# Performance work log

Measured on AMD Instinct MI355X. Metric: run time of the kernel, lower is better.

Reference implementation:

```python
import jax, jax.numpy as jnp
import numpy as np

L, C = 32768, 512
EPS = 1e-5

def _layernorm(x, w, b):
    mu = jnp.mean(x, axis=-1, keepdims=True)
    var = jnp.mean(jnp.square(x - mu), axis=-1, keepdims=True)
    return (x - mu) * jax.lax.rsqrt(var + EPS) * w + b

def _scan(u, decay):
    # inclusive first-order linear scan: b_t = decay * b_{t-1} + u_t
    a = jnp.broadcast_to(decay, u.shape)
    def combine(l, r):
        return (l[0] * r[0], r[1] + r[0] * l[1])
    _, b = jax.lax.associative_scan(combine, (a, u), axis=0)
    return b

def setup_inputs() -> dict:
    key = jax.random.key(0)
    ks = jax.random.split(key, 8)
    s = 0.02
    return {
        "x": jax.random.normal(ks[0], (L, C), dtype=jnp.float32),
        "ln1_w": jnp.ones((C,), jnp.float32),
        "ln1_b": jnp.zeros((C,), jnp.float32),
        "W_in": jax.random.normal(ks[1], (C, C), jnp.float32) * s,
        "b_in": jnp.zeros((C,), jnp.float32),
        "W_gate": jax.random.normal(ks[2], (C, C), jnp.float32) * s,
        "b_gate": jnp.zeros((C,), jnp.float32),
        "W_out": jax.random.normal(ks[3], (C, C), jnp.float32) * s,
        "b_out": jnp.zeros((C,), jnp.float32),
        "decay_logit": jnp.zeros((C,), jnp.float32),  # torch init: zeros -> sigmoid = 0.5
        "ln2_w": jnp.ones((C,), jnp.float32),
        "ln2_b": jnp.zeros((C,), jnp.float32),
        "W_ff1": jax.random.normal(ks[4], (C, 2 * C), jnp.float32) * s,
        "b_ff1": jnp.zeros((2 * C,), jnp.float32),
        "W_ff2": jax.random.normal(ks[5], (2 * C, C), jnp.float32) * s,
        "b_ff2": jnp.zeros((C,), jnp.float32),
    }

def reference(x, ln1_w, ln1_b, W_in, b_in, W_gate, b_gate, W_out, b_out,
              decay_logit, ln2_w, ln2_b, W_ff1, b_ff1, W_ff2, b_ff2):
    hidden = _layernorm(x, ln1_w, ln1_b)
    u = hidden @ W_in + b_in
    gate = jax.nn.sigmoid(hidden @ W_gate + b_gate)
    decay = jax.nn.sigmoid(decay_logit)
    fwd = _scan(u, decay) * gate
    bwd = jnp.flip(_scan(jnp.flip(u, axis=0), decay), axis=0) * gate
    state_out = 0.5 * (fwd + bwd)
    x = x + state_out @ W_out + b_out
    h = _layernorm(x, ln2_w, ln2_b)
    x = x + jax.nn.silu(h @ W_ff1 + b_ff1) @ W_ff2 + b_ff2
    return x
```

## Files before the change

### kernel.cpp

```cpp
#include <hip/hip_runtime.h>
#include <stdint.h>


#define L_SEQ 32768
#define CDIM 512
#define LN_EPS 1e-5f
#define CHUNK 64
#define NCHUNK (L_SEQ / CHUNK)

typedef __attribute__((ext_vector_type(8))) short short8;
typedef __attribute__((ext_vector_type(4))) float floatx4;

__device__ inline unsigned short f2bf(float f) {
  union { float f; unsigned int u; } v; v.f = f;
  unsigned int r = v.u + 0x7fffu + ((v.u >> 16) & 1u);
  return (unsigned short)(r >> 16);
}
__device__ inline float bf2f(unsigned short h) {
  union { float f; unsigned int u; } v; v.u = ((unsigned int)h) << 16;
  return v.f;
}
__device__ inline float sigmoidf_(float x) { return 1.0f / (1.0f + __expf(-x)); }

__device__ __forceinline__ void gll16(const void* g, void* l) {
  __builtin_amdgcn_global_load_lds(
      (__attribute__((address_space(1))) void*)g,
      (__attribute__((address_space(3))) void*)l, 16, 0, 0);
}

__global__ __launch_bounds__(256) void ln_kernel(const float* __restrict__ x,
    const float* __restrict__ w, const float* __restrict__ b,
    unsigned short* __restrict__ out) {
  int row = blockIdx.x * 4 + (threadIdx.x >> 6);
  int lane = threadIdx.x & 63;
  const float4* xr = (const float4*)(x + (size_t)row * CDIM);
  float4 v0 = xr[lane * 2];
  float4 v1 = xr[lane * 2 + 1];
  float s = v0.x + v0.y + v0.z + v0.w + v1.x + v1.y + v1.z + v1.w;
  float s2 = v0.x * v0.x + v0.y * v0.y + v0.z * v0.z + v0.w * v0.w +
             v1.x * v1.x + v1.y * v1.y + v1.z * v1.z + v1.w * v1.w;
  for (int m = 32; m > 0; m >>= 1) {
    s += __shfl_xor(s, m, 64);
    s2 += __shfl_xor(s2, m, 64);
  }
  float mean = s * (1.0f / CDIM);
  float var = s2 * (1.0f / CDIM) - mean * mean;
  float rs = rsqrtf(var + LN_EPS);
  const float4* wr = (const float4*)w;
  const float4* br = (const float4*)b;
  float4 w0 = wr[lane * 2], w1 = wr[lane * 2 + 1];
  float4 b0 = br[lane * 2], b1 = br[lane * 2 + 1];
  unsigned int p0 = (unsigned int)f2bf((v0.x - mean) * rs * w0.x + b0.x) |
                    ((unsigned int)f2bf((v0.y - mean) * rs * w0.y + b0.y) << 16);
  unsigned int p1 = (unsigned int)f2bf((v0.z - mean) * rs * w0.z + b0.z) |
                    ((unsigned int)f2bf((v0.w - mean) * rs * w0.w + b0.w) << 16);
  unsigned int p2 = (unsigned int)f2bf((v1.x - mean) * rs * w1.x + b1.x) |
                    ((unsigned int)f2bf((v1.y - mean) * rs * w1.y + b1.y) << 16);
  unsigned int p3 = (unsigned int)f2bf((v1.z - mean) * rs * w1.z + b1.z) |
                    ((unsigned int)f2bf((v1.w - mean) * rs * w1.w + b1.w) << 16);
  uint4 pk; pk.x = p0; pk.y = p1; pk.z = p2; pk.w = p3;
  *((uint4*)(out + (size_t)row * CDIM + lane * 8)) = pk;
}

__global__ __launch_bounds__(256) void prep_all(
    const float* __restrict__ W_in, const float* __restrict__ W_gate,
    const float* __restrict__ W_out, const float* __restrict__ W_ff1,
    const float* __restrict__ W_ff2, const float* __restrict__ logit,
    unsigned short* __restrict__ Wt_ig, unsigned short* __restrict__ Wt_out,
    unsigned short* __restrict__ Wt_ff1, unsigned short* __restrict__ Wt_ff2,
    float* __restrict__ decay, float* __restrict__ decayT) {
  int b = blockIdx.x;
  if (b >= 1792) {
    for (int c = threadIdx.x; c < CDIM; c += 256) {
      float d = sigmoidf_(logit[c]);
      decay[c] = d;
      float p = d;
      for (int i = 0; i < 6; i++) p *= p;
      decayT[c] = p;
    }
    return;
  }
  const float* W; unsigned short* Wt; int Kd, Nd, t;
  if (b < 256)       { W = W_in;   Wt = Wt_ig;             Kd = 512;  Nd = 512;  t = b; }
  else if (b < 512)  { W = W_gate; Wt = Wt_ig + 512 * 512; Kd = 512;  Nd = 512;  t = b - 256; }
  else if (b < 768)  { W = W_out;  Wt = Wt_out;            Kd = 512;  Nd = 512;  t = b - 512; }
  else if (b < 1280) { W = W_ff1;  Wt = Wt_ff1;            Kd = 512;  Nd = 1024; t = b - 768; }
  else               { W = W_ff2;  Wt = Wt_ff2;            Kd = 1024; Nd = 512;  t = b - 1280; }
  int ntx = Nd >> 5;
  int n0 = (t % ntx) * 32, k0 = (t / ntx) * 32;
  __shared__ float tile[32][33];
  int tx = threadIdx.x & 31, ty = threadIdx.x >> 5;
  for (int r = 0; r < 32; r += 8)
    tile[ty + r][tx] = W[(size_t)(k0 + ty + r) * Nd + n0 + tx];
  __syncthreads();
  for (int r = 0; r < 32; r += 8)
    Wt[(size_t)(n0 + ty + r) * Kd + k0 + tx] = f2bf(tile[tx][ty + r]);
}

template <int EPI>
__global__ __launch_bounds__(512, 2) void gemm256(
    const unsigned short* __restrict__ A, const unsigned short* __restrict__ Bt,
    const float* __restrict__ biasA, const float* __restrict__ biasB,
    const float* __restrict__ res, float* __restrict__ outF,
    unsigned short* __restrict__ outU, unsigned short* __restrict__ outG,
    int M, int N, int K) {
  __shared__ unsigned short smem[65536];
  unsigned short* As = smem;
  unsigned short* Bs = smem + 32768;

  int nbx = gridDim.x, nby = gridDim.y;
  int bid = blockIdx.x + blockIdx.y * nbx;
  int per = (nbx * nby) >> 3;
  int w = (bid & 7) * per + (bid >> 3);
  int ni = w % nby, mi = w / nby;
  int bm = mi << 8, bn = ni << 8;

  int tid = threadIdx.x, wave = tid >> 6, lane = tid & 63;
  int wm = (wave >> 2) * 128, wn = (wave & 3) * 64;
  int quad = lane >> 4, r16 = lane & 15;

  int sr = tid >> 2;
  int sc = tid & 3;
  int swz = (sr >> 1) & 3;
  const unsigned short* aSrc0 = A + (size_t)(bm + sr) * K + ((sc ^ swz) * 8);
  const unsigned short* aSrc1 = aSrc0 + (size_t)128 * K;
  const unsigned short* bSrc0 = Bt + (size_t)(bn + sr) * K + ((sc ^ swz) * 8);
  const unsigned short* bSrc1 = bSrc0 + (size_t)128 * K;
  int ldsW = wave * 512;

#define STAGE(slot, ktile) do {                                   \
    int _o = (ktile) * 32;                                        \
    unsigned short* _a = As + (slot) * 8192 + ldsW;               \
    unsigned short* _b = Bs + (slot) * 8192 + ldsW;               \
    gll16(aSrc0 + _o, _a);                                        \
    gll16(aSrc1 + _o, _a + 4096);                                 \
    gll16(bSrc0 + _o, _b);                                        \
    gll16(bSrc1 + _o, _b + 4096);                                 \
  } while (0)

  floatx4 acc[8][4];
#pragma unroll
  for (int i = 0; i < 8; i++)
#pragma unroll
    for (int j = 0; j < 4; j++) acc[i][j] = (floatx4){0.f, 0.f, 0.f, 0.f};

  int cOff = ((quad ^ ((r16 >> 1) & 3)) & 3) * 8;
  int aBase = (wm + r16) * 32 + cOff;
  int bBase = (wn + r16) * 32 + cOff;

  int NK = K >> 5;

  STAGE(0, 0); STAGE(1, 1); STAGE(2, 2);
  asm volatile("s_waitcnt vmcnt(8)" ::: "memory");
  __builtin_amdgcn_s_barrier();
  asm volatile("" ::: "memory");

  for (int j = 0; j < NK; ++j) {
    int slot = j & 3;
    if (j + 3 < NK) STAGE((j + 3) & 3, j + 3);
    const unsigned short* as = As + slot * 8192;
    const unsigned short* bs = Bs + slot * 8192;
    short8 af[8], bfr[4];
#pragma unroll
    for (int i = 0; i < 8; i++) af[i] = *(const short8*)(as + aBase + i * 512);
#pragma unroll
    for (int jj = 0; jj < 4; jj++) bfr[jj] = *(const short8*)(bs + bBase + jj * 512);
    if (j + 1 < NK) {
      asm volatile("s_waitcnt lgkmcnt(0)" ::: "memory");
      if (j + 3 < NK)      asm volatile("s_waitcnt vmcnt(8)" ::: "memory");
      else if (j + 2 < NK) asm volatile("s_waitcnt vmcnt(4)" ::: "memory");
      else                 asm volatile("s_waitcnt vmcnt(0)" ::: "memory");
      __builtin_amdgcn_s_barrier();
      asm volatile("" ::: "memory");
    }
    __builtin_amdgcn_s_setprio(1);
#pragma unroll
    for (int i = 0; i < 8; i++)
#pragma unroll
      for (int jj = 0; jj < 4; jj++)
        acc[i][jj] = __builtin_amdgcn_mfma_f32_16x16x32_bf16(af[i], bfr[jj], acc[i][jj], 0, 0, 0);
    __builtin_amdgcn_s_setprio(0);
  }
#undef STAGE

  if (EPI == 1) {
#pragma unroll
    for (int i = 0; i < 8; i++) {
      int mb = bm + wm + i * 16 + quad * 4;
#pragma unroll
      for (int jj = 0; jj < 4; jj++) {
        int n = bn + wn + jj * 16 + r16;
        float bA = biasA[n];
#pragma unroll
        for (int r = 0; r < 4; r++) {
          size_t idx = (size_t)(mb + r) * N + n;
          outF[idx] = res[idx] + acc[i][jj][r] + bA;
        }
      }
    }
  } else {
    unsigned short* sm16 = smem;
#define EPI_HALF(P) {                                                        \
      __syncthreads(); \
      _Pragma("unroll")                                                      \
      for (int jj = 0; jj < 4; jj++) {                                       \
        int colL = wn + jj * 16 + r16;                                       \
        int n = bn + colL;                                                   \
        _Pragma("unroll")                                                    \
        for (int i = 0; i < 4; i++) {                                        \
          int lr = (wm >> 1) + i * 16 + quad * 4;                            \
          _Pragma("unroll")                                                  \
          for (int r = 0; r < 4; r++) {                                      \
            float v = acc[(P) * 4 + i][jj][r];                               \
            float t;                                                         \
            if (EPI == 0) {                                                  \
              t = (n < 512) ? (v + biasA[n]) : sigmoidf_(v + biasB[n - 512]);\
            } else {                                           \
              float z = v + biasA[n];                                        \
              t = z * sigmoidf_(z);                                          \
            }                                                                \
            sm16[(lr + r) * 260 + colL] = f2bf(t);                           \
          }                                                                  \
        }                                                                    \
      }                                                                      \
      __syncthreads();                                                       \
      {                                                                      \
        int row = tid >> 2, c0 = (tid & 3) * 64;                             \
        int gr = bm + (row & 63) + ((row >> 6) * 128) + (P) * 64;            \
        const unsigned short* srcp = sm16 + row * 260 + c0;                  \
        unsigned short* gptr;                                                \
        if (EPI == 0) {                                                      \
          gptr = (bn < 512) ? (outU + (size_t)gr * 512 + bn + c0)            \
                            : (outG + (size_t)gr * 512 + (bn - 512) + c0);   \
        } else {                                                             \
          gptr = outG + (size_t)gr * N + bn + c0;                            \
        }                                                                    \
        _Pragma("unroll")                                                    \
        for (int s = 0; s < 8; s++)                                          \
          *(short8*)(gptr + s * 8) = *(const short8*)(srcp + s * 8);         \
      }                                                                      \
    }
    EPI_HALF(0)
    EPI_HALF(1)
#undef EPI_HALF
  }
}

__global__ __launch_bounds__(512) void scan_phase1(const unsigned short* __restrict__ u,
    const float* __restrict__ decay, float* __restrict__ fa, float* __restrict__ ba) {
  int c = threadIdx.x, k = blockIdx.x;
  float d = decay[c];
  const unsigned short* up = u + (size_t)k * CHUNK * CDIM + c;
  float f = 0.f, bs = 0.f, p = 1.f;
#pragma unroll 8
  for (int t = 0; t < CHUNK; t++) {
    float v = bf2f(up[(size_t)t * CDIM]);
    f = d * f + v;
    bs += p * v;
    p *= d;
  }
  fa[(size_t)k * CDIM + c] = f;
  ba[(size_t)k * CDIM + c] = bs;
}

__global__ __launch_bounds__(256) void scan_phase2(const float* __restrict__ fa,
    const float* __restrict__ ba, const float* __restrict__ decayT,
    float* __restrict__ fc, float* __restrict__ bc) {
  int c = blockIdx.x * 256 + threadIdx.x;
  float dT = decayT[c];
  float runf = 0.f, runb = 0.f;
#pragma unroll 4
  for (int k = 0; k < NCHUNK; k++) {
    int kb = NCHUNK - 1 - k;
    fc[(size_t)k * CDIM + c] = runf;
    runf = dT * runf + fa[(size_t)k * CDIM + c];
    bc[(size_t)kb * CDIM + c] = runb;
    runb = dT * runb + ba[(size_t)kb * CDIM + c];
  }
}

__global__ __launch_bounds__(512) void scan_phase3(const unsigned short* __restrict__ u,
    const unsigned short* __restrict__ gate, const float* __restrict__ decay,
    const float* __restrict__ fc, const float* __restrict__ bc,
    unsigned short* __restrict__ state) {
  int c = threadIdx.x, k = blockIdx.x;
  float d = decay[c];
  size_t base = (size_t)k * CHUNK * CDIM + c;
  float fwd[CHUNK];
  float run = fc[(size_t)k * CDIM + c];
#pragma unroll
  for (int t = 0; t < CHUNK; t++) {
    run = d * run + bf2f(u[base + (size_t)t * CDIM]);
    fwd[t] = run;
  }
  float runb = bc[(size_t)k * CDIM + c];
#pragma unroll
  for (int t = CHUNK - 1; t >= 0; t--) {
    runb = d * runb + bf2f(u[base + (size_t)t * CDIM]);
    float g = bf2f(gate[base + (size_t)t * CDIM]);
    state[base + (size_t)t * CDIM] = f2bf(0.5f * (fwd[t] + runb) * g);
  }
}

extern "C" void kernel_launch(void* const* d_in, const int* in_sizes, int n_in,
                              void* d_out, int out_size, void* d_ws, size_t ws_size,
                              hipStream_t stream) {
  const float* x = (const float*)d_in[0];
  const float* ln1_w = (const float*)d_in[1];
  const float* ln1_b = (const float*)d_in[2];
  const float* W_in = (const float*)d_in[3];
  const float* b_in = (const float*)d_in[4];
  const float* W_gate = (const float*)d_in[5];
  const float* b_gate = (const float*)d_in[6];
  const float* W_out = (const float*)d_in[7];
  const float* b_out = (const float*)d_in[8];
  const float* decay_logit = (const float*)d_in[9];
  const float* ln2_w = (const float*)d_in[10];
  const float* ln2_b = (const float*)d_in[11];
  const float* W_ff1 = (const float*)d_in[12];
  const float* b_ff1 = (const float*)d_in[13];
  const float* W_ff2 = (const float*)d_in[14];
  const float* b_ff2 = (const float*)d_in[15];

  char* ws = (char*)d_ws;
  size_t off = 0;
  auto alloc = [&](size_t bytes) -> void* {
    void* p = ws + off;
    off += (bytes + 255) & ~(size_t)255;
    return p;
  };
  unsigned short* Wt_ig  = (unsigned short*)alloc((size_t)1024 * 512 * 2);
  unsigned short* Wt_out = (unsigned short*)alloc((size_t)512 * 512 * 2);
  unsigned short* Wt_ff1 = (unsigned short*)alloc((size_t)1024 * 512 * 2);
  unsigned short* Wt_ff2 = (unsigned short*)alloc((size_t)512 * 1024 * 2);
  float* fa = (float*)alloc((size_t)NCHUNK * CDIM * 4);
  float* ba = (float*)alloc((size_t)NCHUNK * CDIM * 4);
  float* fc = (float*)alloc((size_t)NCHUNK * CDIM * 4);
  float* bc = (float*)alloc((size_t)NCHUNK * CDIM * 4);
  float* decay  = (float*)alloc(CDIM * 4);
  float* decayT = (float*)alloc(CDIM * 4);
  const size_t LC2 = (size_t)L_SEQ * CDIM * 2;
  unsigned short* R1 = (unsigned short*)alloc(LC2);
  unsigned short* R2 = (unsigned short*)alloc(LC2);
  unsigned short* R3 = (unsigned short*)alloc(LC2);
  unsigned short* hidden = R1;
  unsigned short* state  = R1;
  unsigned short* hbuf   = R1;
  unsigned short* u_buf  = R2;
  unsigned short* gate   = R3;
  unsigned short* ffb    = R2;
  float* x2 = (float*)d_out;

  prep_all<<<1793, 256, 0, stream>>>(W_in, W_gate, W_out, W_ff1, W_ff2,
      decay_logit, Wt_ig, Wt_out, Wt_ff1, Wt_ff2, decay, decayT);

  ln_kernel<<<L_SEQ / 4, 256, 0, stream>>>(x, ln1_w, ln1_b, hidden);

  gemm256<0><<<dim3(L_SEQ / 256, 1024 / 256), 512, 0, stream>>>(
      hidden, Wt_ig, b_in, b_gate, nullptr, nullptr, u_buf, gate, L_SEQ, 1024, 512);

  scan_phase1<<<NCHUNK, 512, 0, stream>>>(u_buf, decay, fa, ba);
  scan_phase2<<<2, 256, 0, stream>>>(fa, ba, decayT, fc, bc);
  scan_phase3<<<NCHUNK, 512, 0, stream>>>(u_buf, gate, decay, fc, bc, state);

  gemm256<1><<<dim3(L_SEQ / 256, 512 / 256), 512, 0, stream>>>(
      state, Wt_out, b_out, nullptr, x, x2, nullptr, nullptr, L_SEQ, 512, 512);

  ln_kernel<<<L_SEQ / 4, 256, 0, stream>>>(x2, ln2_w, ln2_b, hbuf);

  gemm256<2><<<dim3(L_SEQ / 256, 1024 / 256), 512, 0, stream>>>(
      hbuf, Wt_ff1, b_ff1, nullptr, nullptr, nullptr, nullptr, ffb, L_SEQ, 1024, 512);

  gemm256<1><<<dim3(L_SEQ / 256, 512 / 256), 512, 0, stream>>>(
      ffb, Wt_ff2, b_ff2, nullptr, x2, x2, nullptr, nullptr, L_SEQ, 512, 1024);
}
```

Before: 462.8 us.

## Interleave LDS reads, global prefetch, and MFMA groups in GEMM main loop

```diff
diff --git a/kernel.cpp b/kernel.cpp
--- a/kernel.cpp
+++ b/kernel.cpp
@@ -10,6 +10,7 @@
 
 typedef __attribute__((ext_vector_type(8))) short short8;
 typedef __attribute__((ext_vector_type(4))) float floatx4;
+typedef __attribute__((ext_vector_type(4))) int intx4;
 
 __device__ inline unsigned short f2bf(float f) {
   union { float f; unsigned int u; } v; v.f = f;
@@ -21,6 +22,9 @@
   return v.f;
 }
 __device__ inline float sigmoidf_(float x) { return 1.0f / (1.0f + __expf(-x)); }
+__device__ __forceinline__ short8 asS8(intx4 v) {
+  union { intx4 i; short8 s; } u; u.i = v; return u.s;
+}
 
 __device__ __forceinline__ void gll16(const void* g, void* l) {
   __builtin_amdgcn_global_load_lds(
@@ -128,7 +132,7 @@
   const unsigned short* bSrc1 = bSrc0 + (size_t)128 * K;
   int ldsW = wave * 512;
 
-#define STAGE(slot, ktile) do {                                   \
+#define STAGE4(slot, ktile) do {                                  \
     int _o = (ktile) * 32;                                        \
     unsigned short* _a = As + (slot) * 8192 + ldsW;               \
     unsigned short* _b = Bs + (slot) * 8192 + ldsW;               \
@@ -145,43 +149,91 @@
     for (int j = 0; j < 4; j++) acc[i][j] = (floatx4){0.f, 0.f, 0.f, 0.f};
 
   int cOff = ((quad ^ ((r16 >> 1) & 3)) & 3) * 8;
-  int aBase = (wm + r16) * 32 + cOff;
-  int bBase = (wn + r16) * 32 + cOff;
+  unsigned aByte = (unsigned)(((wm + r16) * 32 + cOff) * 2);
+  unsigned bByte = 65536u + (unsigned)(((wn + r16) * 32 + cOff) * 2);
 
   int NK = K >> 5;
 
-  STAGE(0, 0); STAGE(1, 1); STAGE(2, 2);
+#define DSR(dst, byteOff) asm volatile("ds_read_b128 %0, %1"              \
+    : "=v"(dst)                                                           \
+    : "v"((__attribute__((address_space(3))) const void*)                 \
+          ((const char*)smem + (byteOff))))
+
+#define LGKM0_FENCE() do {                                                \
+    asm volatile("s_waitcnt lgkmcnt(0)" ::: "memory");                    \
+    __builtin_amdgcn_sched_barrier(0);                                    \
+  } while (0)
+
+#define MFMA8(Q, A0, A1) do {                                             \
+    __builtin_amdgcn_s_setprio(1);                                        \
+    short8 _a0 = asS8(A0), _a1 = asS8(A1);                                \
+    short8 _b0 = asS8(tb0), _b1 = asS8(tb1), _b2 = asS8(tb2), _b3 = asS8(tb3); \
+    acc[2*(Q)  ][0] = __builtin_amdgcn_mfma_f32_16x16x32_bf16(_a0, _b0, acc[2*(Q)  ][0], 0, 0, 0); \
+    acc[2*(Q)  ][1] = __builtin_amdgcn_mfma_f32_16x16x32_bf16(_a0, _b1, acc[2*(Q)  ][1], 0, 0, 0); \
+    acc[2*(Q)  ][2] = __builtin_amdgcn_mfma_f32_16x16x32_bf16(_a0, _b2, acc[2*(Q)  ][2], 0, 0, 0); \
+    acc[2*(Q)  ][3] = __builtin_amdgcn_mfma_f32_16x16x32_bf16(_a0, _b3, acc[2*(Q)  ][3], 0, 0, 0); \
+    acc[2*(Q)+1][0] = __builtin_amdgcn_mfma_f32_16x16x32_bf16(_a1, _b0, acc[2*(Q)+1][0], 0, 0, 0); \
+    acc[2*(Q)+1][1] = __builtin_amdgcn_mfma_f32_16x16x32_bf16(_a1, _b1, acc[2*(Q)+1][1], 0, 0, 0); \
+    acc[2*(Q)+1][2] = __builtin_amdgcn_mfma_f32_16x16x32_bf16(_a1, _b2, acc[2*(Q)+1][2], 0, 0, 0); \
+    acc[2*(Q)+1][3] = __builtin_amdgcn_mfma_f32_16x16x32_bf16(_a1, _b3, acc[2*(Q)+1][3], 0, 0, 0); \
+    __builtin_amdgcn_s_setprio(0);                                        \
+  } while (0)
+
+  STAGE4(0, 0); STAGE4(1, 1); STAGE4(2, 2);
   asm volatile("s_waitcnt vmcnt(8)" ::: "memory");
   __builtin_amdgcn_s_barrier();
-  asm volatile("" ::: "memory");
-
+
+  intx4 tb0, tb1, tb2, tb3;
   for (int j = 0; j < NK; ++j) {
     int slot = j & 3;
-    if (j + 3 < NK) STAGE((j + 3) & 3, j + 3);
-    const unsigned short* as = As + slot * 8192;
-    const unsigned short* bs = Bs + slot * 8192;
-    short8 af[8], bfr[4];
-#pragma unroll
-    for (int i = 0; i < 8; i++) af[i] = *(const short8*)(as + aBase + i * 512);
-#pragma unroll
-    for (int jj = 0; jj < 4; jj++) bfr[jj] = *(const short8*)(bs + bBase + jj * 512);
-    if (j + 1 < NK) {
-      asm volatile("s_waitcnt lgkmcnt(0)" ::: "memory");
-      if (j + 3 < NK)      asm volatile("s_waitcnt vmcnt(8)" ::: "memory");
-      else if (j + 2 < NK) asm volatile("s_waitcnt vmcnt(4)" ::: "memory");
-      else                 asm volatile("s_waitcnt vmcnt(0)" ::: "memory");
-      __builtin_amdgcn_s_barrier();
-      asm volatile("" ::: "memory");
-    }
-    __builtin_amdgcn_s_setprio(1);
-#pragma unroll
-    for (int i = 0; i < 8; i++)
-#pragma unroll
-      for (int jj = 0; jj < 4; jj++)
-        acc[i][jj] = __builtin_amdgcn_mfma_f32_16x16x32_bf16(af[i], bfr[jj], acc[i][jj], 0, 0, 0);
-    __builtin_amdgcn_s_setprio(0);
-  }
-#undef STAGE
+    unsigned so = (unsigned)slot * 16384u;
+    unsigned aA = aByte + so, bA = bByte + so;
+    bool st = (j + 3 < NK);
+    int o3 = (j + 3) * 32;
+    int s3 = (j + 3) & 3;
+    unsigned short* a3 = As + s3 * 8192 + ldsW;
+    unsigned short* b3 = Bs + s3 * 8192 + ldsW;
+
+    intx4 t0, t1;
+    DSR(tb0, bA);
+    DSR(tb1, bA + 1024u);
+    DSR(tb2, bA + 2048u);
+    DSR(tb3, bA + 3072u);
+    DSR(t0, aA);
+    DSR(t1, aA + 1024u);
+    if (st) gll16(aSrc0 + o3, a3);
+    LGKM0_FENCE();
+    MFMA8(0, t0, t1);
+
+    intx4 t2, t3;
+    DSR(t2, aA + 2048u);
+    DSR(t3, aA + 3072u);
+    if (st) gll16(aSrc1 + o3, a3 + 4096);
+    LGKM0_FENCE();
+    MFMA8(1, t2, t3);
+
+    intx4 t4, t5;
+    DSR(t4, aA + 4096u);
+    DSR(t5, aA + 5120u);
+    if (st) gll16(bSrc0 + o3, b3);
+    LGKM0_FENCE();
+    MFMA8(2, t4, t5);
+
+    intx4 t6, t7;
+    DSR(t6, aA + 6144u);
+    DSR(t7, aA + 7168u);
+    if (st) gll16(bSrc1 + o3, b3 + 4096);
+    if (st)                  asm volatile("s_waitcnt vmcnt(8)" ::: "memory");
+    else if (j + 2 < NK)     asm volatile("s_waitcnt vmcnt(4)" ::: "memory");
+    else if (j + 1 < NK)     asm volatile("s_waitcnt vmcnt(0)" ::: "memory");
+    LGKM0_FENCE();
+    MFMA8(3, t6, t7);
+    __builtin_amdgcn_s_barrier();
+  }
+#undef STAGE4
+#undef DSR
+#undef LGKM0_FENCE
+#undef MFMA8
 
   if (EPI == 1) {
 #pragma unroll
```

Measured after the change: 459.7 us. No clear change (-0.7%).
